# Kernel optimization log

Measured on AMD Instinct MI355X. Metric: run time of the kernel, lower is better.

The kernel has to match this reference:

```python
import jax, jax.numpy as jnp
import numpy as np

NUM_HEADS = 16
DIM_K = 64
EMB_DIM = 1024
NEG_INF = -1.0e9


def setup_inputs() -> dict:
    key = jax.random.key(0)
    ks = jax.random.split(key, 12)
    B, Sq, Skv, D = 2, 2048, 2048, EMB_DIM
    HDK = NUM_HEADS * DIM_K
    s = 1.0 / np.sqrt(D)
    return {
        "q": jax.random.normal(ks[0], (B, Sq, D), jnp.float32),
        "k": jax.random.normal(ks[1], (B, Skv, D), jnp.float32),
        "v": jax.random.normal(ks[2], (B, Skv, D), jnp.float32),
        "mask": jax.random.randint(ks[3], (B, 1, Skv), 0, 2, jnp.int32),
        "Wq": jax.random.normal(ks[4], (D, HDK), jnp.float32) * s,
        "bq": jnp.zeros((HDK,), jnp.float32),
        "Wk": jax.random.normal(ks[5], (D, HDK), jnp.float32) * s,
        "bk": jnp.zeros((HDK,), jnp.float32),
        "Wv": jax.random.normal(ks[6], (D, HDK), jnp.float32) * s,
        "bv": jnp.zeros((HDK,), jnp.float32),
        "Wo": jax.random.normal(ks[7], (HDK, D), jnp.float32) * (1.0 / np.sqrt(HDK)),
        "bo": jnp.zeros((D,), jnp.float32),
    }


def reference(q, k, v, mask, Wq, bq, Wk, bk, Wv, bv, Wo, bo):
    B, Sq, _ = q.shape
    Skv = k.shape[1]
    H, dk = NUM_HEADS, DIM_K
    # projections  (B,S,D) -> (B,H,S,dk)
    qh = (q @ Wq + bq).reshape(B, Sq, H, dk).transpose(0, 2, 1, 3)
    kh = (k @ Wk + bk).reshape(B, Skv, H, dk).transpose(0, 2, 1, 3)
    vh = (v @ Wv + bv).reshape(B, Skv, H, dk).transpose(0, 2, 1, 3)
    # scores (B,H,Sq,Skv)
    scores = jnp.einsum("bhqd,bhkd->bhqk", qh, kh) / jnp.float32(np.sqrt(dk))
    # mask (B,1,Skv) -> (B,1,1,Skv); masked_fill where mask == 0
    scores = jnp.where(mask[:, None] == 0, jnp.float32(NEG_INF), scores)
    probs = jax.nn.softmax(scores, axis=-1)  # dropout is identity in eval
    attn = jnp.einsum("bhqk,bhkd->bhqd", probs, vh)
    concat = attn.transpose(0, 2, 1, 3).reshape(B, Sq, H * dk)
    output = concat @ Wo + bo
    return output, scores
```

## Files before the change

kernel.cpp:

```cpp
#include <hip/hip_runtime.h>
#include <hip/hip_bf16.h>

typedef __attribute__((ext_vector_type(8))) short short8;
typedef __attribute__((ext_vector_type(4))) float f32x4;
typedef __hip_bfloat16 bf16;

typedef const void __attribute__((address_space(1))) as1_const_void;
typedef void __attribute__((address_space(3))) as3_void;

static __device__ __forceinline__ void gload_lds16(const bf16* g, bf16* l) {
    __builtin_amdgcn_global_load_lds((as1_const_void*)g, (as3_void*)l, 16, 0, 0);
}

#define NH 16
#define DK 64
#define SEQ 2048
#define DIM 1024
#define NEG_INF_F (-1.0e9f)

static __device__ __forceinline__ unsigned short f2bf_bits(float f) {
    bf16 t = __float2bfloat16(f);
    return *reinterpret_cast<unsigned short*>(&t);
}

__global__ void cvt_all_kernel(const float* __restrict__ q, const float* __restrict__ k,
                               const float* __restrict__ v, bf16* __restrict__ qb,
                               bf16* __restrict__ kb, bf16* __restrict__ vb) {
    const int N4 = 2 * SEQ * DIM / 4;
    int i = blockIdx.x * blockDim.x + threadIdx.x;
    int sel = i / N4, j = i - sel * N4;
    const float* in = (sel == 0) ? q : (sel == 1) ? k : v;
    bf16* out = (sel == 0) ? qb : (sel == 1) ? kb : vb;
    float4 x = reinterpret_cast<const float4*>(in)[j];
    ushort4 u;
    u.x = f2bf_bits(x.x);
    u.y = f2bf_bits(x.y);
    u.z = f2bf_bits(x.z);
    u.w = f2bf_bits(x.w);
    reinterpret_cast<ushort4*>(out)[j] = u;
}

__global__ void transpose_cvt_kernel(const float* __restrict__ Wq, const float* __restrict__ Wk,
                                     const float* __restrict__ Wv, const float* __restrict__ Wo,
                                     bf16* __restrict__ Wqt, bf16* __restrict__ Wkt,
                                     bf16* __restrict__ Wvt, bf16* __restrict__ Wot) {
    __shared__ float t[32][33];
    const int z = blockIdx.z;
    const float* W = (z == 0) ? Wq : (z == 1) ? Wk : (z == 2) ? Wv : Wo;
    bf16* Wt = (z == 0) ? Wqt : (z == 1) ? Wkt : (z == 2) ? Wvt : Wot;
    int n0 = blockIdx.x * 32, k0 = blockIdx.y * 32;
    int tx = threadIdx.x, ty = threadIdx.y;
#pragma unroll
    for (int i = 0; i < 4; i++)
        t[ty + i * 8][tx] = W[(size_t)(k0 + ty + i * 8) * DIM + n0 + tx];
    __syncthreads();
#pragma unroll
    for (int i = 0; i < 4; i++)
        Wt[(size_t)(n0 + ty + i * 8) * DIM + k0 + tx] = __float2bfloat16(t[tx][ty + i * 8]);
}

__global__ __launch_bounds__(256) void qkv_gemm_kernel(
    const bf16* __restrict__ qb, const bf16* __restrict__ kb, const bf16* __restrict__ vb,
    const bf16* __restrict__ Wcat,
    const float* __restrict__ bq, const float* __restrict__ bk, const float* __restrict__ bv,
    bf16* __restrict__ Qh, bf16* __restrict__ Kh, bf16* __restrict__ Vt)
{
    __shared__ __align__(16) bf16 Xs[2][128 * 32];
    __shared__ __align__(16) bf16 Ws[2][128 * 32];
    const int tid = threadIdx.x;
    const int w = tid >> 6, l = tid & 63;
    const int l15 = l & 15, l4 = l >> 4;
    const int lin = blockIdx.x;
    const int swz = (lin & 7) * 96 + (lin >> 3);
    const int proj = swz >> 8;
    const int rem = swz & 255;
    const int m0 = (rem >> 3) * 128;
    const int n0 = (rem & 7) * 128;
    const bf16* X = (proj == 0) ? qb : (proj == 1) ? kb : vb;
    const bf16* Wt = Wcat + (size_t)proj * DIM * DIM + (size_t)n0 * DIM;
    const float* bias = (proj == 0) ? bq : (proj == 1) ? bk : bv;
    const int wr = w >> 1, wc = w & 1;
    f32x4 acc[4][4] = {};

    const int c0 = tid, c1 = 256 + tid;
    const int r0 = c0 >> 2, ch0 = c0 & 3;
    const int r1 = c1 >> 2, ch1 = c1 & 3;
    const bf16* Xp = X + (size_t)m0 * DIM;

    gload_lds16(&Xp[(size_t)r0 * DIM + ch0 * 8], &Xs[0][c0 * 8]);
    gload_lds16(&Xp[(size_t)r1 * DIM + ch1 * 8], &Xs[0][c1 * 8]);
    gload_lds16(&Wt[(size_t)r0 * DIM + ch0 * 8], &Ws[0][c0 * 8]);
    gload_lds16(&Wt[(size_t)r1 * DIM + ch1 * 8], &Ws[0][c1 * 8]);
    __syncthreads();

    int cur = 0;
    for (int k0 = 0; k0 < DIM; k0 += 32) {
        if (k0 + 32 < DIM) {
            gload_lds16(&Xp[(size_t)r0 * DIM + k0 + 32 + ch0 * 8], &Xs[cur ^ 1][c0 * 8]);
            gload_lds16(&Xp[(size_t)r1 * DIM + k0 + 32 + ch1 * 8], &Xs[cur ^ 1][c1 * 8]);
            gload_lds16(&Wt[(size_t)r0 * DIM + k0 + 32 + ch0 * 8], &Ws[cur ^ 1][c0 * 8]);
            gload_lds16(&Wt[(size_t)r1 * DIM + k0 + 32 + ch1 * 8], &Ws[cur ^ 1][c1 * 8]);
        }
        short8 af[4], bfr[4];
#pragma unroll
        for (int mi = 0; mi < 4; mi++)
            af[mi] = *reinterpret_cast<const short8*>(&Xs[cur][(wr * 64 + mi * 16 + l15) * 32 + l4 * 8]);
#pragma unroll
        for (int ni = 0; ni < 4; ni++)
            bfr[ni] = *reinterpret_cast<const short8*>(&Ws[cur][(wc * 64 + ni * 16 + l15) * 32 + l4 * 8]);
#pragma unroll
        for (int mi = 0; mi < 4; mi++)
#pragma unroll
            for (int ni = 0; ni < 4; ni++)
                acc[mi][ni] = __builtin_amdgcn_mfma_f32_16x16x32_bf16(af[mi], bfr[ni], acc[mi][ni], 0, 0, 0);
        __syncthreads();
        cur ^= 1;
    }

#pragma unroll
    for (int mi = 0; mi < 4; mi++) {
#pragma unroll
        for (int ni = 0; ni < 4; ni++) {
            int n = n0 + wc * 64 + ni * 16 + l15;
            float bv = bias[n];
            int h = n >> 6, d = n & 63;
#pragma unroll
            for (int j = 0; j < 4; j++) {
                int m = m0 + wr * 64 + mi * 16 + l4 * 4 + j;
                float val = acc[mi][ni][j] + bv;
                int b = m >> 11, s = m & 2047;
                if (proj == 0)
                    Qh[((size_t)(b * NH + h) * SEQ + s) * DK + d] = __float2bfloat16(val * 0.125f);
                else if (proj == 1)
                    Kh[((size_t)(b * NH + h) * SEQ + s) * DK + d] = __float2bfloat16(val);
                else
                    Vt[((size_t)(b * NH + h) * DK + d) * SEQ + s] = __float2bfloat16(val);
            }
        }
    }
}

__global__ __launch_bounds__(256) void o_gemm_kernel(
    const bf16* __restrict__ X, const bf16* __restrict__ Wt,
    const float* __restrict__ bias, float* __restrict__ out)
{
    __shared__ __align__(16) bf16 Xs[2][64 * 32];
    __shared__ __align__(16) bf16 Ws[2][128 * 32];
    const int tid = threadIdx.x;
    const int w = tid >> 6, l = tid & 63;
    const int l15 = l & 15, l4 = l >> 4;
    const int lin = blockIdx.x;
    const int swz = (lin & 7) * 64 + (lin >> 3);
    const int m0 = (swz >> 3) * 64;
    const int n0 = (swz & 7) * 128;
    const int wr = w >> 1, wc = w & 1;
    f32x4 acc[2][4] = {};

    const int c0 = tid, c1 = 256 + tid;
    const int r0 = c0 >> 2, ch0 = c0 & 3;
    const int r1 = c1 >> 2, ch1 = c1 & 3;
    const bf16* Xp = X + (size_t)m0 * DIM;
    const bf16* Wp = Wt + (size_t)n0 * DIM;

    gload_lds16(&Xp[(size_t)r0 * DIM + ch0 * 8], &Xs[0][c0 * 8]);
    gload_lds16(&Wp[(size_t)r0 * DIM + ch0 * 8], &Ws[0][c0 * 8]);
    gload_lds16(&Wp[(size_t)r1 * DIM + ch1 * 8], &Ws[0][c1 * 8]);
    __syncthreads();

    int cur = 0;
    for (int k0 = 0; k0 < DIM; k0 += 32) {
        if (k0 + 32 < DIM) {
            gload_lds16(&Xp[(size_t)r0 * DIM + k0 + 32 + ch0 * 8], &Xs[cur ^ 1][c0 * 8]);
            gload_lds16(&Wp[(size_t)r0 * DIM + k0 + 32 + ch0 * 8], &Ws[cur ^ 1][c0 * 8]);
            gload_lds16(&Wp[(size_t)r1 * DIM + k0 + 32 + ch1 * 8], &Ws[cur ^ 1][c1 * 8]);
        }
        short8 af[2], bfr[4];
#pragma unroll
        for (int mi = 0; mi < 2; mi++)
            af[mi] = *reinterpret_cast<const short8*>(&Xs[cur][(wr * 32 + mi * 16 + l15) * 32 + l4 * 8]);
#pragma unroll
        for (int ni = 0; ni < 4; ni++)
            bfr[ni] = *reinterpret_cast<const short8*>(&Ws[cur][(wc * 64 + ni * 16 + l15) * 32 + l4 * 8]);
#pragma unroll
        for (int mi = 0; mi < 2; mi++)
#pragma unroll
            for (int ni = 0; ni < 4; ni++)
                acc[mi][ni] = __builtin_amdgcn_mfma_f32_16x16x32_bf16(af[mi], bfr[ni], acc[mi][ni], 0, 0, 0);
        __syncthreads();
        cur ^= 1;
    }

#pragma unroll
    for (int mi = 0; mi < 2; mi++) {
#pragma unroll
        for (int ni = 0; ni < 4; ni++) {
            int n = n0 + wc * 64 + ni * 16 + l15;
            float bv = bias[n];
#pragma unroll
            for (int j = 0; j < 4; j++) {
                int m = m0 + wr * 32 + mi * 16 + l4 * 4 + j;
                out[(size_t)m * DIM + n] = acc[mi][ni][j] + bv;
            }
        }
    }
}

__global__ __launch_bounds__(256) void attn_kernel(
    const bf16* __restrict__ Qh, const bf16* __restrict__ Kh,
    const bf16* __restrict__ Vt, const int* __restrict__ mask,
    float* __restrict__ scores, bf16* __restrict__ attn_c)
{
    __shared__ __align__(16) bf16 Ks[2][64 * 72];
    __shared__ __align__(16) bf16 Vs[2][64 * 72];
    __shared__ __align__(16) bf16 Ps[128 * 72];
    __shared__ int msk_s[SEQ];
    const int tid = threadIdx.x;
    const int w = tid >> 6, l = tid & 63;
    const int l15 = l & 15, l4 = l >> 4;
    const int lin = blockIdx.x;
    const int swz = (lin & 7) * 64 + (lin >> 3);
    const int bh = swz >> 4;
    const int q0 = (swz & 15) * 128;
    const int b = bh >> 4, h = bh & 15;
    const size_t head = (size_t)bh * SEQ * DK;

    const int c0 = tid, c1 = 256 + tid;
    const int kr0 = c0 >> 3, kc0 = c0 & 7;
    const int kr1 = c1 >> 3, kc1 = c1 & 7;

    short8 aq[2][2];
#pragma unroll
    for (int mi = 0; mi < 2; mi++)
#pragma unroll
        for (int ks = 0; ks < 2; ks++)
            aq[mi][ks] = *reinterpret_cast<const short8*>(
                &Qh[head + (size_t)(q0 + w * 32 + mi * 16 + l15) * DK + ks * 32 + l4 * 8]);

    {
        const int4* msrc = reinterpret_cast<const int4*>(mask + b * SEQ);
#pragma unroll
        for (int i = 0; i < 2; i++)
            reinterpret_cast<int4*>(msk_s)[i * 256 + tid] = msrc[i * 256 + tid];
        short8 k0v = *reinterpret_cast<const short8*>(&Kh[head + (size_t)kr0 * DK + kc0 * 8]);
        short8 k1v = *reinterpret_cast<const short8*>(&Kh[head + (size_t)kr1 * DK + kc1 * 8]);
        short8 v0v = *reinterpret_cast<const short8*>(&Vt[head + (size_t)kr0 * SEQ + kc0 * 8]);
        short8 v1v = *reinterpret_cast<const short8*>(&Vt[head + (size_t)kr1 * SEQ + kc1 * 8]);
        *reinterpret_cast<short8*>(&Ks[0][kr0 * 72 + kc0 * 8]) = k0v;
        *reinterpret_cast<short8*>(&Ks[0][kr1 * 72 + kc1 * 8]) = k1v;
        *reinterpret_cast<short8*>(&Vs[0][kr0 * 72 + kc0 * 8]) = v0v;
        *reinterpret_cast<short8*>(&Vs[0][kr1 * 72 + kc1 * 8]) = v1v;
    }
    __syncthreads();

    f32x4 oacc[2][4] = {};
    float mrun[2][4], lrun[2][4];
#pragma unroll
    for (int mi = 0; mi < 2; mi++)
#pragma unroll
        for (int j = 0; j < 4; j++) { mrun[mi][j] = -INFINITY; lrun[mi][j] = 0.f; }

    int cur = 0;
    for (int t = 0; t < SEQ / 64; t++) {
        const int kv0 = t * 64;
        const bool more = t < (SEQ / 64 - 1);
        short8 nk0, nk1, nv0, nv1;
        if (more) {
            nk0 = *reinterpret_cast<const short8*>(&Kh[head + (size_t)(kv0 + 64 + kr0) * DK + kc0 * 8]);
            nk1 = *reinterpret_cast<const short8*>(&Kh[head + (size_t)(kv0 + 64 + kr1) * DK + kc1 * 8]);
            nv0 = *reinterpret_cast<const short8*>(&Vt[head + (size_t)kr0 * SEQ + kv0 + 64 + kc0 * 8]);
            nv1 = *reinterpret_cast<const short8*>(&Vt[head + (size_t)kr1 * SEQ + kv0 + 64 + kc1 * 8]);
        }

        f32x4 sacc[2][4] = {};
#pragma unroll
        for (int ks = 0; ks < 2; ks++) {
            short8 bk[4];
#pragma unroll
            for (int ni = 0; ni < 4; ni++)
                bk[ni] = *reinterpret_cast<const short8*>(&Ks[cur][(ni * 16 + l15) * 72 + ks * 32 + l4 * 8]);
#pragma unroll
            for (int mi = 0; mi < 2; mi++)
#pragma unroll
                for (int ni = 0; ni < 4; ni++)
                    sacc[mi][ni] = __builtin_amdgcn_mfma_f32_16x16x32_bf16(aq[mi][ks], bk[ni], sacc[mi][ni], 0, 0, 0);
        }

        int mk[4];
#pragma unroll
        for (int ni = 0; ni < 4; ni++) mk[ni] = msk_s[kv0 + ni * 16 + l15];
#pragma unroll
        for (int mi = 0; mi < 2; mi++)
#pragma unroll
            for (int ni = 0; ni < 4; ni++)
                if (mk[ni] == 0) {
#pragma unroll
                    for (int j = 0; j < 4; j++) sacc[mi][ni][j] = NEG_INF_F;
                }

        {
            size_t base = ((size_t)bh * SEQ + q0 + w * 32) * SEQ + kv0;
#pragma unroll
            for (int mi = 0; mi < 2; mi++)
#pragma unroll
                for (int j = 0; j < 4; j++) {
                    size_t rb = base + (size_t)(mi * 16 + l4 * 4 + j) * SEQ;
#pragma unroll
                    for (int ni = 0; ni < 4; ni++)
                        __builtin_nontemporal_store(sacc[mi][ni][j], &scores[rb + ni * 16 + l15]);
                }
        }

#pragma unroll
        for (int mi = 0; mi < 2; mi++)
#pragma unroll
            for (int j = 0; j < 4; j++) {
                float mx = fmaxf(fmaxf(sacc[mi][0][j], sacc[mi][1][j]),
                                 fmaxf(sacc[mi][2][j], sacc[mi][3][j]));
#pragma unroll
                for (int d = 1; d < 16; d <<= 1) mx = fmaxf(mx, __shfl_xor(mx, d));
                if (mx > mrun[mi][j]) {
                    float fac = __expf(mrun[mi][j] - mx);
                    lrun[mi][j] *= fac;
#pragma unroll
                    for (int ni = 0; ni < 4; ni++) oacc[mi][ni][j] *= fac;
                    mrun[mi][j] = mx;
                }
                float mcur = mrun[mi][j];
                float ps = 0.f;
#pragma unroll
                for (int ni = 0; ni < 4; ni++) {
                    float p = __expf(sacc[mi][ni][j] - mcur);
                    sacc[mi][ni][j] = p;
                    ps += p;
                }
                lrun[mi][j] += ps;
            }

#pragma unroll
        for (int mi = 0; mi < 2; mi++)
#pragma unroll
            for (int j = 0; j < 4; j++) {
                int r = w * 32 + mi * 16 + l4 * 4 + j;
#pragma unroll
                for (int ni = 0; ni < 4; ni++)
                    Ps[r * 72 + ni * 16 + l15] = __float2bfloat16(sacc[mi][ni][j]);
            }

#pragma unroll
        for (int ks = 0; ks < 2; ks++) {
            short8 pa[2], vbf[4];
#pragma unroll
            for (int mi = 0; mi < 2; mi++)
                pa[mi] = *reinterpret_cast<const short8*>(&Ps[(w * 32 + mi * 16 + l15) * 72 + ks * 32 + l4 * 8]);
#pragma unroll
            for (int ni = 0; ni < 4; ni++)
                vbf[ni] = *reinterpret_cast<const short8*>(&Vs[cur][(ni * 16 + l15) * 72 + ks * 32 + l4 * 8]);
#pragma unroll
            for (int mi = 0; mi < 2; mi++)
#pragma unroll
                for (int ni = 0; ni < 4; ni++)
                    oacc[mi][ni] = __builtin_amdgcn_mfma_f32_16x16x32_bf16(pa[mi], vbf[ni], oacc[mi][ni], 0, 0, 0);
        }

        if (more) {
            *reinterpret_cast<short8*>(&Ks[cur ^ 1][kr0 * 72 + kc0 * 8]) = nk0;
            *reinterpret_cast<short8*>(&Ks[cur ^ 1][kr1 * 72 + kc1 * 8]) = nk1;
            *reinterpret_cast<short8*>(&Vs[cur ^ 1][kr0 * 72 + kc0 * 8]) = nv0;
            *reinterpret_cast<short8*>(&Vs[cur ^ 1][kr1 * 72 + kc1 * 8]) = nv1;
        }
        __syncthreads();
        cur ^= 1;
    }

#pragma unroll
    for (int mi = 0; mi < 2; mi++)
#pragma unroll
        for (int j = 0; j < 4; j++) {
            float ls = lrun[mi][j];
#pragma unroll
            for (int d = 1; d < 16; d <<= 1) ls += __shfl_xor(ls, d);
            float inv = 1.f / ls;
            int s = q0 + w * 32 + mi * 16 + l4 * 4 + j;
#pragma unroll
            for (int ni = 0; ni < 4; ni++)
                attn_c[((size_t)(b * SEQ + s)) * DIM + h * DK + ni * 16 + l15] =
                    __float2bfloat16(oacc[mi][ni][j] * inv);
        }
}

extern "C" void kernel_launch(void* const* d_in, const int* in_sizes, int n_in,
                              void* d_out, int out_size, void* d_ws, size_t ws_size,
                              hipStream_t stream)
{
    const float* q  = (const float*)d_in[0];
    const float* k  = (const float*)d_in[1];
    const float* v  = (const float*)d_in[2];
    const int*  msk = (const int*)d_in[3];
    const float* Wq = (const float*)d_in[4];
    const float* bq = (const float*)d_in[5];
    const float* Wk = (const float*)d_in[6];
    const float* bk = (const float*)d_in[7];
    const float* Wv = (const float*)d_in[8];
    const float* bv = (const float*)d_in[9];
    const float* Wo = (const float*)d_in[10];
    const float* bo = (const float*)d_in[11];

    const size_t MB = 1ull << 20;
    char* ws = (char*)d_ws;
    bf16* qb  = (bf16*)(ws + 0 * MB);
    bf16* kb  = (bf16*)(ws + 8 * MB);
    bf16* vb  = (bf16*)(ws + 16 * MB);
    bf16* Wqt = (bf16*)(ws + 24 * MB);
    bf16* Wkt = (bf16*)(ws + 26 * MB);
    bf16* Wvt = (bf16*)(ws + 28 * MB);
    bf16* Wot = (bf16*)(ws + 30 * MB);
    bf16* QhD = (bf16*)(ws + 32 * MB);
    bf16* KhD = (bf16*)(ws + 40 * MB);
    bf16* VtD = (bf16*)(ws + 48 * MB);
    bf16* att = (bf16*)(ws + 56 * MB);

    float* out = (float*)d_out;
    float* scores = out + (size_t)4096 * 1024;

    cvt_all_kernel<<<3 * 4096, 256, 0, stream>>>(q, k, v, qb, kb, vb);
    transpose_cvt_kernel<<<dim3(32, 32, 4), dim3(32, 8), 0, stream>>>(
        Wq, Wk, Wv, Wo, Wqt, Wkt, Wvt, Wot);

    qkv_gemm_kernel<<<768, 256, 0, stream>>>(qb, kb, vb, Wqt, bq, bk, bv, QhD, KhD, VtD);

    attn_kernel<<<512, 256, 0, stream>>>(QhD, KhD, VtD, msk, scores, att);

    o_gemm_kernel<<<512, 256, 0, stream>>>(att, Wot, bo, out);
}
```

Before: 242.0 us.

## Split attention KV range across two blocks and merge partial softmax results

Each attention block now processes half of the key/value sequence, which doubles the grid to 1024 blocks. Unnormalized partial outputs and per-row (max, sum) pairs are written to workspace, and a new merge kernel combines them into the concatenated attention output. The K/V LDS buffers go from double to single buffering, the shared mask copy is replaced by direct global reads, and launch bounds are raised to three blocks per CU, all to improve occupancy. A lazy rescale skips the max reduction and rescaling when the new tile's max stays within a threshold of the running max. The cost is an extra kernel launch, partial outputs stored in bf16 before the merge, and an extra barrier per iteration.

```diff
diff --git a/kernel.cpp b/kernel.cpp
--- a/kernel.cpp
+++ b/kernel.cpp
@@ -205,29 +205,34 @@
     }
 }
 
-__global__ __launch_bounds__(256) void attn_kernel(
+__global__ __launch_bounds__(256, 3) void attn_kernel(
     const bf16* __restrict__ Qh, const bf16* __restrict__ Kh,
     const bf16* __restrict__ Vt, const int* __restrict__ mask,
-    float* __restrict__ scores, bf16* __restrict__ attn_c)
+    float* __restrict__ scores, bf16* __restrict__ Op, float2* __restrict__ ml)
 {
-    __shared__ __align__(16) bf16 Ks[2][64 * 72];
-    __shared__ __align__(16) bf16 Vs[2][64 * 72];
+    __shared__ __align__(16) bf16 Ks[64 * 72];
+    __shared__ __align__(16) bf16 Vs[64 * 72];
     __shared__ __align__(16) bf16 Ps[128 * 72];
-    __shared__ int msk_s[SEQ];
     const int tid = threadIdx.x;
     const int w = tid >> 6, l = tid & 63;
     const int l15 = l & 15, l4 = l >> 4;
     const int lin = blockIdx.x;
-    const int swz = (lin & 7) * 64 + (lin >> 3);
-    const int bh = swz >> 4;
+    const int swz = (lin & 7) * 128 + (lin >> 3);
+    const int bh = swz >> 5;
+    const int half = (swz >> 4) & 1;
     const int q0 = (swz & 15) * 128;
     const int b = bh >> 4, h = bh & 15;
     const size_t head = (size_t)bh * SEQ * DK;
+    const int hbase = half * (SEQ / 2);
 
     const int c0 = tid, c1 = 256 + tid;
     const int kr0 = c0 >> 3, kc0 = c0 & 7;
     const int kr1 = c1 >> 3, kc1 = c1 & 7;
 
+    const bf16* Kp = Kh + head;
+    const bf16* Vp = Vt + head;
+    const int* mrow = mask + b * SEQ;
+
     short8 aq[2][2];
 #pragma unroll
     for (int mi = 0; mi < 2; mi++)
@@ -237,18 +242,14 @@
                 &Qh[head + (size_t)(q0 + w * 32 + mi * 16 + l15) * DK + ks * 32 + l4 * 8]);
 
     {
-        const int4* msrc = reinterpret_cast<const int4*>(mask + b * SEQ);
-#pragma unroll
-        for (int i = 0; i < 2; i++)
-            reinterpret_cast<int4*>(msk_s)[i * 256 + tid] = msrc[i * 256 + tid];
-        short8 k0v = *reinterpret_cast<const short8*>(&Kh[head + (size_t)kr0 * DK + kc0 * 8]);
-        short8 k1v = *reinterpret_cast<const short8*>(&Kh[head + (size_t)kr1 * DK + kc1 * 8]);
-        short8 v0v = *reinterpret_cast<const short8*>(&Vt[head + (size_t)kr0 * SEQ + kc0 * 8]);
-        short8 v1v = *reinterpret_cast<const short8*>(&Vt[head + (size_t)kr1 * SEQ + kc1 * 8]);
-        *reinterpret_cast<short8*>(&Ks[0][kr0 * 72 + kc0 * 8]) = k0v;
-        *reinterpret_cast<short8*>(&Ks[0][kr1 * 72 + kc1 * 8]) = k1v;
-        *reinterpret_cast<short8*>(&Vs[0][kr0 * 72 + kc0 * 8]) = v0v;
-        *reinterpret_cast<short8*>(&Vs[0][kr1 * 72 + kc1 * 8]) = v1v;
+        short8 k0v = *reinterpret_cast<const short8*>(&Kp[(size_t)(hbase + kr0) * DK + kc0 * 8]);
+        short8 k1v = *reinterpret_cast<const short8*>(&Kp[(size_t)(hbase + kr1) * DK + kc1 * 8]);
+        short8 v0v = *reinterpret_cast<const short8*>(&Vp[(size_t)kr0 * SEQ + hbase + kc0 * 8]);
+        short8 v1v = *reinterpret_cast<const short8*>(&Vp[(size_t)kr1 * SEQ + hbase + kc1 * 8]);
+        *reinterpret_cast<short8*>(&Ks[kr0 * 72 + kc0 * 8]) = k0v;
+        *reinterpret_cast<short8*>(&Ks[kr1 * 72 + kc1 * 8]) = k1v;
+        *reinterpret_cast<short8*>(&Vs[kr0 * 72 + kc0 * 8]) = v0v;
+        *reinterpret_cast<short8*>(&Vs[kr1 * 72 + kc1 * 8]) = v1v;
     }
     __syncthreads();
 
@@ -259,16 +260,15 @@
 #pragma unroll
         for (int j = 0; j < 4; j++) { mrun[mi][j] = -INFINITY; lrun[mi][j] = 0.f; }
 
-    int cur = 0;
-    for (int t = 0; t < SEQ / 64; t++) {
-        const int kv0 = t * 64;
-        const bool more = t < (SEQ / 64 - 1);
+    for (int t = 0; t < SEQ / 128; t++) {
+        const int kv0 = hbase + t * 64;
+        const bool more = t < (SEQ / 128 - 1);
         short8 nk0, nk1, nv0, nv1;
         if (more) {
-            nk0 = *reinterpret_cast<const short8*>(&Kh[head + (size_t)(kv0 + 64 + kr0) * DK + kc0 * 8]);
-            nk1 = *reinterpret_cast<const short8*>(&Kh[head + (size_t)(kv0 + 64 + kr1) * DK + kc1 * 8]);
-            nv0 = *reinterpret_cast<const short8*>(&Vt[head + (size_t)kr0 * SEQ + kv0 + 64 + kc0 * 8]);
-            nv1 = *reinterpret_cast<const short8*>(&Vt[head + (size_t)kr1 * SEQ + kv0 + 64 + kc1 * 8]);
+            nk0 = *reinterpret_cast<const short8*>(&Kp[(size_t)(kv0 + 64 + kr0) * DK + kc0 * 8]);
+            nk1 = *reinterpret_cast<const short8*>(&Kp[(size_t)(kv0 + 64 + kr1) * DK + kc1 * 8]);
+            nv0 = *reinterpret_cast<const short8*>(&Vp[(size_t)kr0 * SEQ + kv0 + 64 + kc0 * 8]);
+            nv1 = *reinterpret_cast<const short8*>(&Vp[(size_t)kr1 * SEQ + kv0 + 64 + kc1 * 8]);
         }
 
         f32x4 sacc[2][4] = {};
@@ -277,7 +277,7 @@
             short8 bk[4];
 #pragma unroll
             for (int ni = 0; ni < 4; ni++)
-                bk[ni] = *reinterpret_cast<const short8*>(&Ks[cur][(ni * 16 + l15) * 72 + ks * 32 + l4 * 8]);
+                bk[ni] = *reinterpret_cast<const short8*>(&Ks[(ni * 16 + l15) * 72 + ks * 32 + l4 * 8]);
 #pragma unroll
             for (int mi = 0; mi < 2; mi++)
 #pragma unroll
@@ -287,7 +287,7 @@
 
         int mk[4];
 #pragma unroll
-        for (int ni = 0; ni < 4; ni++) mk[ni] = msk_s[kv0 + ni * 16 + l15];
+        for (int ni = 0; ni < 4; ni++) mk[ni] = mrow[kv0 + ni * 16 + l15];
 #pragma unroll
         for (int mi = 0; mi < 2; mi++)
 #pragma unroll
@@ -310,21 +310,37 @@
                 }
         }
 
+        float pmax[2][4];
+        int ok = 1;
 #pragma unroll
         for (int mi = 0; mi < 2; mi++)
 #pragma unroll
             for (int j = 0; j < 4; j++) {
-                float mx = fmaxf(fmaxf(sacc[mi][0][j], sacc[mi][1][j]),
-                                 fmaxf(sacc[mi][2][j], sacc[mi][3][j]));
-#pragma unroll
-                for (int d = 1; d < 16; d <<= 1) mx = fmaxf(mx, __shfl_xor(mx, d));
-                if (mx > mrun[mi][j]) {
-                    float fac = __expf(mrun[mi][j] - mx);
-                    lrun[mi][j] *= fac;
-#pragma unroll
-                    for (int ni = 0; ni < 4; ni++) oacc[mi][ni][j] *= fac;
-                    mrun[mi][j] = mx;
+                pmax[mi][j] = fmaxf(fmaxf(sacc[mi][0][j], sacc[mi][1][j]),
+                                    fmaxf(sacc[mi][2][j], sacc[mi][3][j]));
+                ok &= (pmax[mi][j] <= mrun[mi][j] + 8.f) ? 1 : 0;
+            }
+        if (!__all(ok)) {
+#pragma unroll
+            for (int mi = 0; mi < 2; mi++)
+#pragma unroll
+                for (int j = 0; j < 4; j++) {
+                    float mx = pmax[mi][j];
+#pragma unroll
+                    for (int d = 1; d < 16; d <<= 1) mx = fmaxf(mx, __shfl_xor(mx, d));
+                    if (mx > mrun[mi][j]) {
+                        float fac = __expf(mrun[mi][j] - mx);
+                        lrun[mi][j] *= fac;
+#pragma unroll
+                        for (int ni = 0; ni < 4; ni++) oacc[mi][ni][j] *= fac;
+                        mrun[mi][j] = mx;
+                    }
                 }
+        }
+#pragma unroll
+        for (int mi = 0; mi < 2; mi++)
+#pragma unroll
+            for (int j = 0; j < 4; j++) {
                 float mcur = mrun[mi][j];
                 float ps = 0.f;
 #pragma unroll
@@ -354,7 +370,7 @@
                 pa[mi] = *reinterpret_cast<const short8*>(&Ps[(w * 32 + mi * 16 + l15) * 72 + ks * 32 + l4 * 8]);
 #pragma unroll
             for (int ni = 0; ni < 4; ni++)
-                vbf[ni] = *reinterpret_cast<const short8*>(&Vs[cur][(ni * 16 + l15) * 72 + ks * 32 + l4 * 8]);
+                vbf[ni] = *reinterpret_cast<const short8*>(&Vs[(ni * 16 + l15) * 72 + ks * 32 + l4 * 8]);
 #pragma unroll
             for (int mi = 0; mi < 2; mi++)
 #pragma unroll
@@ -362,14 +378,14 @@
                     oacc[mi][ni] = __builtin_amdgcn_mfma_f32_16x16x32_bf16(pa[mi], vbf[ni], oacc[mi][ni], 0, 0, 0);
         }
 
+        __syncthreads();
         if (more) {
-            *reinterpret_cast<short8*>(&Ks[cur ^ 1][kr0 * 72 + kc0 * 8]) = nk0;
-            *reinterpret_cast<short8*>(&Ks[cur ^ 1][kr1 * 72 + kc1 * 8]) = nk1;
-            *reinterpret_cast<short8*>(&Vs[cur ^ 1][kr0 * 72 + kc0 * 8]) = nv0;
-            *reinterpret_cast<short8*>(&Vs[cur ^ 1][kr1 * 72 + kc1 * 8]) = nv1;
+            *reinterpret_cast<short8*>(&Ks[kr0 * 72 + kc0 * 8]) = nk0;
+            *reinterpret_cast<short8*>(&Ks[kr1 * 72 + kc1 * 8]) = nk1;
+            *reinterpret_cast<short8*>(&Vs[kr0 * 72 + kc0 * 8]) = nv0;
+            *reinterpret_cast<short8*>(&Vs[kr1 * 72 + kc1 * 8]) = nv1;
         }
         __syncthreads();
-        cur ^= 1;
     }
 
 #pragma unroll
@@ -379,13 +395,42 @@
             float ls = lrun[mi][j];
 #pragma unroll
             for (int d = 1; d < 16; d <<= 1) ls += __shfl_xor(ls, d);
-            float inv = 1.f / ls;
-            int s = q0 + w * 32 + mi * 16 + l4 * 4 + j;
-#pragma unroll
-            for (int ni = 0; ni < 4; ni++)
-                attn_c[((size_t)(b * SEQ + s)) * DIM + h * DK + ni * 16 + l15] =
-                    __float2bfloat16(oacc[mi][ni][j] * inv);
-        }
+            int rg = bh * SEQ + q0 + w * 32 + mi * 16 + l4 * 4 + j;
+            if (l15 == 0) {
+                float2 r;
+                r.x = mrun[mi][j];
+                r.y = ls;
+                ml[(half << 16) + rg] = r;
+            }
+            size_t ob = ((size_t)half << 16) * DK + (size_t)rg * DK;
+#pragma unroll
+            for (int ni = 0; ni < 4; ni++)
+                Op[ob + ni * 16 + l15] = __float2bfloat16(oacc[mi][ni][j]);
+        }
+}
+
+__global__ void merge_kernel(const bf16* __restrict__ Op, const float2* __restrict__ ml,
+                             bf16* __restrict__ att) {
+    int gid = blockIdx.x * 256 + threadIdx.x;
+    int r = gid >> 3, c = gid & 7;
+    float2 p0 = ml[r], p1 = ml[65536 + r];
+    float M = fmaxf(p0.x, p1.x);
+    float f0 = __expf(p0.x - M), f1 = __expf(p1.x - M);
+    float inv = 1.f / (p0.y * f0 + p1.y * f1);
+    short8 o0 = *reinterpret_cast<const short8*>(&Op[(size_t)r * DK + c * 8]);
+    short8 o1 = *reinterpret_cast<const short8*>(&Op[(size_t)65536 * DK + (size_t)r * DK + c * 8]);
+    short8 res;
+#pragma unroll
+    for (int i = 0; i < 8; i++) {
+        unsigned short u0 = (unsigned short)o0[i], u1 = (unsigned short)o1[i];
+        float a = __bfloat162float(*reinterpret_cast<bf16*>(&u0));
+        float bb = __bfloat162float(*reinterpret_cast<bf16*>(&u1));
+        bf16 t = __float2bfloat16((a * f0 + bb * f1) * inv);
+        res[i] = *reinterpret_cast<short*>(&t);
+    }
+    int bh = r >> 11, s = r & 2047;
+    int b = bh >> 4, h = bh & 15;
+    *reinterpret_cast<short8*>(&att[((size_t)(b * SEQ + s)) * DIM + h * DK + c * 8]) = res;
 }
 
 extern "C" void kernel_launch(void* const* d_in, const int* in_sizes, int n_in,
@@ -418,6 +463,8 @@
     bf16* KhD = (bf16*)(ws + 40 * MB);
     bf16* VtD = (bf16*)(ws + 48 * MB);
     bf16* att = (bf16*)(ws + 56 * MB);
+    bf16* Op  = (bf16*)(ws + 0 * MB);
+    float2* ml = (float2*)(ws + 18 * MB);
 
     float* out = (float*)d_out;
     float* scores = out + (size_t)4096 * 1024;
@@ -428,7 +475,8 @@
 
     qkv_gemm_kernel<<<768, 256, 0, stream>>>(qb, kb, vb, Wqt, bq, bk, bv, QhD, KhD, VtD);
 
-    attn_kernel<<<512, 256, 0, stream>>>(QhD, KhD, VtD, msk, scores, att);
+    attn_kernel<<<1024, 256, 0, stream>>>(QhD, KhD, VtD, msk, scores, Op, ml);
+    merge_kernel<<<2048, 256, 0, stream>>>(Op, ml, att);
 
     o_gemm_kernel<<<512, 256, 0, stream>>>(att, Wot, bo, out);
 }
```

Result: slower. 291.9 us (+20.6%).
